# Kernel tuning notes

Hardware: AMD Instinct MI355X
Metric: run time of the kernel (lower is better)

Reference implementation:

```python
import jax, jax.numpy as jnp
import numpy as np

PATCH_SIZE = 16
HOP_DISTANCE = 7.0


def setup_inputs() -> dict:
    key = jax.random.key(0)
    x = jax.random.normal(key, (1, 1024, 1024), dtype=jnp.float32)
    return {"x": x}


def _patchify(x, p):
    # Faithful replication of F.unfold(kernel=p, stride=p) followed by .view(-1, p, p)
    # on the contiguous [1, C*p*p, L] unfold output (row-major reshape).
    C, H, W = x.shape
    nH, nW = H // p, W // p
    # unfold layout: [C*p*p, L] with element (c*p*p + ki*p + kj, bi*nW + bj)
    cols = x.reshape(C, nH, p, nW, p).transpose(0, 2, 4, 1, 3).reshape(C * p * p, nH * nW)
    # torch .view(-1, p, p) on contiguous [C*p*p, L] == row-major reshape
    return cols.reshape(-1, p, p)  # [N, p, p], N = C * nH * nW


def reference(x):
    p = PATCH_SIZE
    patches = _patchify(x, p)  # [N, p, p]
    # distance(patch_i, patch_j) = norm over dim=1 (rows) -> per-column vector of length p.
    # d2[i, j, k] = sum_r (patches[i, r, k] - patches[j, r, k])**2, via Gram trick.
    sq = jnp.sum(patches * patches, axis=1)                      # [N, p]
    G = jnp.einsum('irk,jrk->ijk', patches, patches)             # [N, N, p]
    d2 = jnp.maximum(sq[:, None, :] + sq[None, :, :] - 2.0 * G, 0.0)
    # A[i, j] = 1 iff all per-column norms <= hop_distance
    A = jnp.all(jnp.sqrt(d2) <= HOP_DISTANCE, axis=-1).astype(jnp.float32)  # [N, N]
    return A
```

## Files before the change

kernel.cpp:

```cpp
#include <hip/hip_runtime.h>


#define NPATCH 4096
#define BT 64

__global__ __launch_bounds__(256) void transpose_kernel(const float* __restrict__ x,
                                                        float* __restrict__ P2) {
    int gid = blockIdx.x * 256 + threadIdx.x;
    int nl = gid & 15;
    int c  = (gid >> 4) & 3;
    int n8 = (gid >> 6) & 15;
    int r  = (gid >> 10) & 15;
    int k  = gid >> 14;
    int h = nl * 64 + (r >> 2) * 16 + n8;
    int w0 = (r & 3) * 256 + k * 16 + 4 * c;
    float4 v = *(const float4*)&x[h * 1024 + w0];
    const float* vp = (const float*)&v;
    float* dst = P2 + (((k * 16 + r) << 12) | (n8 << 8) | nl);
#pragma unroll
    for (int j = 0; j < 4; ++j)
        dst[(4 * c + j) << 4] = vp[j];
}

__global__ __launch_bounds__(256) void sq2_kernel(const float* __restrict__ P2,
                                                  float* __restrict__ sq) {
#pragma clang fp contract(off)
    int gid = blockIdx.x * 256 + threadIdx.x;
    int n = gid & 4095;
    int k = gid >> 12;
    const float* p = P2 + ((k * 16) << 12) + n;
    float v0 = p[0];
    float acc = v0 * v0;
#pragma unroll
    for (int r = 1; r < 16; ++r) {
        float v = p[r << 12];
        float t = v * v;
        acc = acc + t;
    }
    sq[(k << 12) + n] = acc;
}

__global__ __launch_bounds__(256, 3) void adj4_kernel(const float* __restrict__ P2,
                                                      const float* __restrict__ sq,
                                                      float* __restrict__ A) {
#pragma clang fp contract(off)
    __shared__ float4 S[2][2][16][16];

    int t = blockIdx.x;
    int bi = (int)((sqrtf(8.0f * (float)t + 1.0f) - 1.0f) * 0.5f);
    while ((bi + 1) * (bi + 2) / 2 <= t) ++bi;
    while (bi * (bi + 1) / 2 > t) --bi;
    int bj = t - bi * (bi + 1) / 2;

    const int i0 = bi * BT;
    const int j0 = bj * BT;
    const int tid = threadIdx.x;
    const int tx = tid & 15;
    const int ty = tid >> 4;
    const int ia = i0 + 4 * ty;
    const int ja = j0 + 4 * tx;

    unsigned int bad = 0u;

    for (int kp = 0; kp < 8; ++kp) {
        __syncthreads();
#pragma unroll
        for (int l = 0; l < 4; ++l) {
            int gid = l * 256 + tid;
            int c = gid & 15;
            int r = (gid >> 4) & 15;
            int kl = (gid >> 8) & 1;
            int side = gid >> 9;
            int k = kp * 2 + kl;
            float4 v = *(const float4*)&P2[(((k << 4) | r) << 12) + (side ? j0 : i0) + 4 * c];
            S[side][kl][r][c] = v;
        }
        __syncthreads();
#pragma unroll
        for (int kl = 0; kl < 2; ++kl) {
            int k = kp * 2 + kl;
            float d[4][4];
#pragma unroll
            for (int u = 0; u < 4; ++u)
#pragma unroll
                for (int v = 0; v < 4; ++v) d[u][v] = 0.0f;
#pragma unroll
            for (int r = 0; r < 16; ++r) {
                float4 a4 = S[0][kl][r][ty];
                float4 b4 = S[1][kl][r][tx];
                const float* ap = (const float*)&a4;
                const float* bp = (const float*)&b4;
#pragma unroll
                for (int u = 0; u < 4; ++u)
#pragma unroll
                    for (int v = 0; v < 4; ++v)
                        d[u][v] = fmaf(ap[u], bp[v], d[u][v]);
            }
            float4 si4 = *(const float4*)&sq[(k << 12) + ia];
            float4 sj4 = *(const float4*)&sq[(k << 12) + ja];
            const float* sip = (const float*)&si4;
            const float* sjp = (const float*)&sj4;
#pragma unroll
            for (int u = 0; u < 4; ++u)
#pragma unroll
                for (int v = 0; v < 4; ++v) {
                    float s = sip[u] + sjp[v];
                    float d2 = fmaf(-2.0f, d[u][v], s);
                    bad |= (d2 > 49.0f) ? (1u << (u * 4 + v)) : 0u;
                }
        }
    }

#pragma unroll
    for (int u = 0; u < 4; ++u) {
        float4 o;
        o.x = (bad >> (u * 4 + 0)) & 1u ? 0.0f : 1.0f;
        o.y = (bad >> (u * 4 + 1)) & 1u ? 0.0f : 1.0f;
        o.z = (bad >> (u * 4 + 2)) & 1u ? 0.0f : 1.0f;
        o.w = (bad >> (u * 4 + 3)) & 1u ? 0.0f : 1.0f;
        *(float4*)&A[(size_t)(i0 + ty * 4 + u) * NPATCH + j0 + tx * 4] = o;
    }
    if (bi != bj) {
#pragma unroll
        for (int v = 0; v < 4; ++v) {
            float4 o;
            o.x = (bad >> (0 * 4 + v)) & 1u ? 0.0f : 1.0f;
            o.y = (bad >> (1 * 4 + v)) & 1u ? 0.0f : 1.0f;
            o.z = (bad >> (2 * 4 + v)) & 1u ? 0.0f : 1.0f;
            o.w = (bad >> (3 * 4 + v)) & 1u ? 0.0f : 1.0f;
            *(float4*)&A[(size_t)(j0 + tx * 4 + v) * NPATCH + i0 + ty * 4] = o;
        }
    }
}


#define KC 2
#define NPH 8
#define RSTRIDE 9

__device__ __forceinline__ int swzrow(int row) {
    return ((row >> 2) + (row >> 5)) & 7;
}

__global__ __launch_bounds__(256, 3) void adj_kernel(const float* __restrict__ x,
                                                     float* __restrict__ A) {
#pragma clang fp contract(off)
    __shared__ float4 Si[BT * RSTRIDE];
    __shared__ float4 Sj[BT * RSTRIDE];
    __shared__ float sqs[2][KC][BT];

    int t = blockIdx.x;
    int bi = (int)((sqrtf(8.0f * (float)t + 1.0f) - 1.0f) * 0.5f);
    while ((bi + 1) * (bi + 2) / 2 <= t) ++bi;
    while (bi * (bi + 1) / 2 > t) --bi;
    int bj = t - bi * (bi + 1) / 2;

    const int i0 = bi * BT;
    const int j0 = bj * BT;
    const int tid = threadIdx.x;
    const int tx = tid & 15;
    const int ty = tid >> 4;
    const int swzA = (ty + (ty >> 3)) & 7;
    const int swzB = (tx + (tx >> 3)) & 7;

    float m[4][4];
#pragma unroll
    for (int u = 0; u < 4; ++u)
#pragma unroll
        for (int v = 0; v < 4; ++v) m[u][v] = -3.0e38f;

    for (int kp = 0; kp < NPH; ++kp) {
        __syncthreads();
#pragma unroll
        for (int l = 0; l < 4; ++l) {
            int gid = l * 256 + tid;
            int side = gid >> 9;
            int q = gid & 511;
            int kl = q & 1;
            int r = (q >> 1) & 15;
            int rl = q >> 5;
            int k = kp * KC + kl;
            int b = side ? bj : bi;
            int h = rl * 64 + (r >> 2) * 16 + (b >> 2);
            int w0 = (r & 3) * 256 + k * 16 + ((4 * b) & 15);
            float4 v = *(const float4*)&x[h * 1024 + w0];
            const float* vp = (const float*)&v;
            int c = (kl << 2) | (r >> 2);
            int e = r & 3;
            float* Sb = side ? (float*)Sj : (float*)Si;
#pragma unroll
            for (int dd = 0; dd < 4; ++dd) {
                int row = 16 * dd + rl;
                int ch = c ^ swzrow(row);
                Sb[(row * RSTRIDE + ch) * 4 + e] = vp[dd];
            }
        }
        __syncthreads();
        {
            int side = tid >> 7;
            int kl = (tid >> 6) & 1;
            int row = tid & 63;
            const float4* Sb = (side ? Sj : Si) + row * RSTRIDE;
            int swz = swzrow(row);
            float acc;
            {
                float4 v = Sb[(kl * 4) ^ swz];
                acc = v.x * v.x;
                float t1 = v.y * v.y; acc = acc + t1;
                float t2 = v.z * v.z; acc = acc + t2;
                float t3 = v.w * v.w; acc = acc + t3;
            }
#pragma unroll
            for (int rc = 1; rc < 4; ++rc) {
                float4 v = Sb[(kl * 4 + rc) ^ swz];
                float t0 = v.x * v.x; acc = acc + t0;
                float t1 = v.y * v.y; acc = acc + t1;
                float t2 = v.z * v.z; acc = acc + t2;
                float t3 = v.w * v.w; acc = acc + t3;
            }
            sqs[side][kl][row] = acc;
        }
        __syncthreads();
#pragma unroll
        for (int kl = 0; kl < KC; ++kl) {
            float d[4][4];
#pragma unroll
            for (int u = 0; u < 4; ++u)
#pragma unroll
                for (int v = 0; v < 4; ++v) d[u][v] = 0.0f;
#pragma unroll
            for (int rc = 0; rc < 4; ++rc) {
                int c = kl * 4 + rc;
                float4 a[4], b[4];
#pragma unroll
                for (int u = 0; u < 4; ++u)
                    a[u] = Si[(ty * 4 + u) * RSTRIDE + (c ^ swzA)];
#pragma unroll
                for (int v = 0; v < 4; ++v)
                    b[v] = Sj[(tx * 4 + v) * RSTRIDE + (c ^ swzB)];
#pragma unroll
                for (int u = 0; u < 4; ++u)
#pragma unroll
                    for (int v = 0; v < 4; ++v) {
                        d[u][v] = fmaf(a[u].x, b[v].x, d[u][v]);
                        d[u][v] = fmaf(a[u].y, b[v].y, d[u][v]);
                        d[u][v] = fmaf(a[u].z, b[v].z, d[u][v]);
                        d[u][v] = fmaf(a[u].w, b[v].w, d[u][v]);
                    }
            }
            float4 si4 = *(const float4*)&sqs[0][kl][ty * 4];
            float4 sj4 = *(const float4*)&sqs[1][kl][tx * 4];
            const float* sip = (const float*)&si4;
            const float* sjp = (const float*)&sj4;
#pragma unroll
            for (int u = 0; u < 4; ++u)
#pragma unroll
                for (int v = 0; v < 4; ++v) {
                    float s = sip[u] + sjp[v];
                    float d2 = fmaf(-2.0f, d[u][v], s);
                    m[u][v] = fmaxf(m[u][v], d2);
                }
        }
    }

#pragma unroll
    for (int u = 0; u < 4; ++u) {
        float4 o;
        o.x = (m[u][0] <= 49.0f) ? 1.0f : 0.0f;
        o.y = (m[u][1] <= 49.0f) ? 1.0f : 0.0f;
        o.z = (m[u][2] <= 49.0f) ? 1.0f : 0.0f;
        o.w = (m[u][3] <= 49.0f) ? 1.0f : 0.0f;
        *(float4*)&A[(size_t)(i0 + ty * 4 + u) * NPATCH + j0 + tx * 4] = o;
    }
    if (bi != bj) {
#pragma unroll
        for (int v = 0; v < 4; ++v) {
            float4 o;
            o.x = (m[0][v] <= 49.0f) ? 1.0f : 0.0f;
            o.y = (m[1][v] <= 49.0f) ? 1.0f : 0.0f;
            o.z = (m[2][v] <= 49.0f) ? 1.0f : 0.0f;
            o.w = (m[3][v] <= 49.0f) ? 1.0f : 0.0f;
            *(float4*)&A[(size_t)(j0 + tx * 4 + v) * NPATCH + i0 + ty * 4] = o;
        }
    }
}

extern "C" void kernel_launch(void* const* d_in, const int* in_sizes, int n_in,
                              void* d_out, int out_size, void* d_ws, size_t ws_size,
                              hipStream_t stream) {
    const float* x = (const float*)d_in[0];
    float* A = (float*)d_out;

    const int nblk = (NPATCH / BT) * (NPATCH / BT + 1) / 2;
    const size_t need = (size_t)4 * 1024 * 1024 + 256 * 1024;

    if (ws_size >= need) {
        float* P2 = (float*)d_ws;
        float* sq = (float*)((char*)d_ws + (size_t)4 * 1024 * 1024);
        transpose_kernel<<<1024, 256, 0, stream>>>(x, P2);
        sq2_kernel<<<256, 256, 0, stream>>>(P2, sq);
        adj4_kernel<<<nblk, 256, 0, stream>>>(P2, sq, A);
    } else {
        adj_kernel<<<nblk, 256, 0, stream>>>(x, A);
    }
}
```

Baseline: 167.3 us.

## Load i-side patch rows from global memory, keep max-distance accumulators, raise occupancy

The i-side operand is no longer staged in shared memory. Each thread reads its float4 straight from global memory (where it is broadcast or cached across the row of threads), which halves LDS use per block. The per-element bitmask is replaced by a running fmaxf of d2 that is thresholded once at the end. Launch bounds go from 3 to 5 blocks, trading registers for occupancy. The risk is extra global/L1 latency in the inner loop and register pressure from the 16 max accumulators.

```diff
diff --git a/kernel.cpp b/kernel.cpp
--- a/kernel.cpp
+++ b/kernel.cpp
@@ -40,11 +40,11 @@
     sq[(k << 12) + n] = acc;
 }
 
-__global__ __launch_bounds__(256, 3) void adj4_kernel(const float* __restrict__ P2,
+__global__ __launch_bounds__(256, 5) void adj5_kernel(const float* __restrict__ P2,
                                                       const float* __restrict__ sq,
                                                       float* __restrict__ A) {
 #pragma clang fp contract(off)
-    __shared__ float4 S[2][2][16][16];
+    __shared__ float4 Sj[2][16][16];
 
     int t = blockIdx.x;
     int bi = (int)((sqrtf(8.0f * (float)t + 1.0f) - 1.0f) * 0.5f);
@@ -60,34 +60,37 @@
     const int ia = i0 + 4 * ty;
     const int ja = j0 + 4 * tx;
 
-    unsigned int bad = 0u;
+    float m[4][4];
+#pragma unroll
+    for (int u = 0; u < 4; ++u)
+#pragma unroll
+        for (int v = 0; v < 4; ++v) m[u][v] = -3.0e38f;
 
     for (int kp = 0; kp < 8; ++kp) {
         __syncthreads();
 #pragma unroll
-        for (int l = 0; l < 4; ++l) {
+        for (int l = 0; l < 2; ++l) {
             int gid = l * 256 + tid;
             int c = gid & 15;
             int r = (gid >> 4) & 15;
-            int kl = (gid >> 8) & 1;
-            int side = gid >> 9;
+            int kl = gid >> 8;
             int k = kp * 2 + kl;
-            float4 v = *(const float4*)&P2[(((k << 4) | r) << 12) + (side ? j0 : i0) + 4 * c];
-            S[side][kl][r][c] = v;
+            Sj[kl][r][c] = *(const float4*)&P2[(((k << 4) | r) << 12) + j0 + 4 * c];
         }
         __syncthreads();
 #pragma unroll
         for (int kl = 0; kl < 2; ++kl) {
             int k = kp * 2 + kl;
+            const float* baseA = P2 + (((size_t)k << 4) << 12) + ia;
             float d[4][4];
 #pragma unroll
             for (int u = 0; u < 4; ++u)
 #pragma unroll
                 for (int v = 0; v < 4; ++v) d[u][v] = 0.0f;
-#pragma unroll
+#pragma unroll 4
             for (int r = 0; r < 16; ++r) {
-                float4 a4 = S[0][kl][r][ty];
-                float4 b4 = S[1][kl][r][tx];
+                float4 a4 = *(const float4*)&baseA[r << 12];
+                float4 b4 = Sj[kl][r][tx];
                 const float* ap = (const float*)&a4;
                 const float* bp = (const float*)&b4;
 #pragma unroll
@@ -106,7 +109,7 @@
                 for (int v = 0; v < 4; ++v) {
                     float s = sip[u] + sjp[v];
                     float d2 = fmaf(-2.0f, d[u][v], s);
-                    bad |= (d2 > 49.0f) ? (1u << (u * 4 + v)) : 0u;
+                    m[u][v] = fmaxf(m[u][v], d2);
                 }
         }
     }
@@ -114,20 +117,20 @@
 #pragma unroll
     for (int u = 0; u < 4; ++u) {
         float4 o;
-        o.x = (bad >> (u * 4 + 0)) & 1u ? 0.0f : 1.0f;
-        o.y = (bad >> (u * 4 + 1)) & 1u ? 0.0f : 1.0f;
-        o.z = (bad >> (u * 4 + 2)) & 1u ? 0.0f : 1.0f;
-        o.w = (bad >> (u * 4 + 3)) & 1u ? 0.0f : 1.0f;
+        o.x = (m[u][0] <= 49.0f) ? 1.0f : 0.0f;
+        o.y = (m[u][1] <= 49.0f) ? 1.0f : 0.0f;
+        o.z = (m[u][2] <= 49.0f) ? 1.0f : 0.0f;
+        o.w = (m[u][3] <= 49.0f) ? 1.0f : 0.0f;
         *(float4*)&A[(size_t)(i0 + ty * 4 + u) * NPATCH + j0 + tx * 4] = o;
     }
     if (bi != bj) {
 #pragma unroll
         for (int v = 0; v < 4; ++v) {
             float4 o;
-            o.x = (bad >> (0 * 4 + v)) & 1u ? 0.0f : 1.0f;
-            o.y = (bad >> (1 * 4 + v)) & 1u ? 0.0f : 1.0f;
-            o.z = (bad >> (2 * 4 + v)) & 1u ? 0.0f : 1.0f;
-            o.w = (bad >> (3 * 4 + v)) & 1u ? 0.0f : 1.0f;
+            o.x = (m[0][v] <= 49.0f) ? 1.0f : 0.0f;
+            o.y = (m[1][v] <= 49.0f) ? 1.0f : 0.0f;
+            o.z = (m[2][v] <= 49.0f) ? 1.0f : 0.0f;
+            o.w = (m[3][v] <= 49.0f) ? 1.0f : 0.0f;
             *(float4*)&A[(size_t)(j0 + tx * 4 + v) * NPATCH + i0 + ty * 4] = o;
         }
     }
@@ -299,7 +302,7 @@
         float* sq = (float*)((char*)d_ws + (size_t)4 * 1024 * 1024);
         transpose_kernel<<<1024, 256, 0, stream>>>(x, P2);
         sq2_kernel<<<256, 256, 0, stream>>>(P2, sq);
-        adj4_kernel<<<nblk, 256, 0, stream>>>(P2, sq, A);
+        adj5_kernel<<<nblk, 256, 0, stream>>>(P2, sq, A);
     } else {
         adj_kernel<<<nblk, 256, 0, stream>>>(x, A);
     }
```

After: 187.4 us. 1.12x slower.
